# Performance work log

Measured on AMD Instinct MI355X. Metric: run time of the kernel, lower is better.

Reference implementation:

```python
import jax, jax.numpy as jnp
import numpy as np
import itertools

DIM = 576; HEADS = 18; HD = 32; WS = 7; H = 28; W = 28; EPS = 1e-5

def _bias_idxs(ws):
    pts = list(itertools.product(range(ws), range(ws)))
    offs = {}
    idxs = []
    for p1 in pts:
        for p2 in pts:
            o = (abs(p1[0] - p2[0]), abs(p1[1] - p2[1]))
            if o not in offs:
                offs[o] = len(offs)
            idxs.append(offs[o])
    return np.array(idxs, np.int32).reshape(len(pts), len(pts))

BIAS_IDXS = _bias_idxs(WS)          # [49, 49]
N_OFF = int(BIAS_IDXS.max()) + 1    # 49 distinct offsets

def _ln(x, g, b):
    m = x.mean(-1, keepdims=True)
    v = ((x - m) ** 2).mean(-1, keepdims=True)
    return (x - m) * jax.lax.rsqrt(v + EPS) * g + b

def setup_inputs() -> dict:
    key = jax.random.key(0)
    ks = jax.random.split(key, 10)
    B = 32; L = H * W; C = DIM; hid = 4 * C
    s = 0.02
    return {
        'x': jax.random.normal(ks[0], (B, L, C), jnp.float32),
        'ln1_g': jnp.ones((C,), jnp.float32),
        'ln1_b': jnp.zeros((C,), jnp.float32),
        'qkv_w': jax.random.normal(ks[1], (C, 3 * C), jnp.float32) * s,
        'qkv_b': jnp.zeros((3 * C,), jnp.float32),
        'attn_biases': jax.random.normal(ks[2], (HEADS, N_OFF), jnp.float32) * s,
        'proj_w': jax.random.normal(ks[3], (C, C), jnp.float32) * s,
        'proj_b': jnp.zeros((C,), jnp.float32),
        'conv_w': jax.random.normal(ks[4], (C, 1, 3, 3), jnp.float32) * 0.1,
        'bn_g': jnp.ones((C,), jnp.float32),
        'bn_b': jnp.zeros((C,), jnp.float32),
        'bn_mean': jax.random.normal(ks[5], (C,), jnp.float32) * 0.1,
        'bn_var': jax.random.uniform(ks[6], (C,), jnp.float32, 0.5, 1.5),
        'ln2_g': jnp.ones((C,), jnp.float32),
        'ln2_b': jnp.zeros((C,), jnp.float32),
        'fc1_w': jax.random.normal(ks[7], (C, hid), jnp.float32) * s,
        'fc1_b': jnp.zeros((hid,), jnp.float32),
        'fc2_w': jax.random.normal(ks[8], (hid, C), jnp.float32) * s,
        'fc2_b': jnp.zeros((C,), jnp.float32),
    }

def reference(x, ln1_g, ln1_b, qkv_w, qkv_b, attn_biases, proj_w, proj_b,
              conv_w, bn_g, bn_b, bn_mean, bn_var, ln2_g, ln2_b,
              fc1_w, fc1_b, fc2_w, fc2_b):
    B, L, C = x.shape
    nH, nW = H // WS, W // WS
    Nw = WS * WS
    scale = HD ** -0.5
    res = x
    # window partition: [B,L,C] -> [B*nH*nW, WS*WS, C] (H,W divisible by WS -> no pad)
    xw = x.reshape(B, nH, WS, nW, WS, C).transpose(0, 1, 3, 2, 4, 5).reshape(-1, Nw, C)
    h = _ln(xw, ln1_g, ln1_b)
    qkv = (h @ qkv_w + qkv_b).reshape(-1, Nw, HEADS, 3 * HD)
    q, k, v = qkv[..., :HD], qkv[..., HD:2 * HD], qkv[..., 2 * HD:]
    bias = attn_biases[:, BIAS_IDXS]  # gather -> [HEADS, Nw, Nw]
    scores = jnp.einsum('bnhd,bmhd->bhnm', q, k) * scale + bias[None]
    a = jax.nn.softmax(scores, axis=-1)
    o = jnp.einsum('bhnm,bmhd->bnhd', a, v).reshape(-1, Nw, C)
    o = o @ proj_w + proj_b
    # window reverse
    o = o.reshape(B, nH, nW, WS, WS, C).transpose(0, 1, 3, 2, 4, 5).reshape(B, L, C)
    x = res + o
    # depthwise 3x3 conv + BatchNorm (eval mode, running stats)
    xc = x.transpose(0, 2, 1).reshape(B, C, H, W)
    y = jax.lax.conv_general_dilated(xc, conv_w, (1, 1), ((1, 1), (1, 1)),
                                     feature_group_count=C,
                                     dimension_numbers=('NCHW', 'OIHW', 'NCHW'))
    inv = jax.lax.rsqrt(bn_var + EPS)
    y = (y - bn_mean[None, :, None, None]) * (inv * bn_g)[None, :, None, None] + bn_b[None, :, None, None]
    x = y.reshape(B, C, L).transpose(0, 2, 1)
    # MLP with pre-LayerNorm (exact GELU, matching torch nn.GELU)
    hm = _ln(x, ln2_g, ln2_b)
    hm = jax.nn.gelu(hm @ fc1_w + fc1_b, approximate=False)
    x = x + (hm @ fc2_w + fc2_b)
    return x
```

## Files before the change

kernel.cpp:

```cpp
#include <hip/hip_runtime.h>
#include <hip/hip_bf16.h>

typedef __attribute__((ext_vector_type(8))) short bf16x8;
typedef __attribute__((ext_vector_type(4))) float f32x4;

static __device__ __forceinline__ void stf(float* p, size_t i, float v) { p[i] = v; }
static __device__ __forceinline__ void stf(__hip_bfloat16* p, size_t i, float v) { p[i] = __float2bfloat16(v); }

static __device__ __forceinline__ void gload_lds16(const void* g, void* l) {
  __builtin_amdgcn_global_load_lds((const __attribute__((address_space(1))) void*)g,
                                   (__attribute__((address_space(3))) void*)l, 16, 0, 0);
}

__global__ void wt_kernel(const float* __restrict__ W, __hip_bfloat16* __restrict__ WT, int K, int N) {
  __shared__ float tile[32][33];
  const int kb = blockIdx.y * 32, nb = blockIdx.x * 32;
  const int tx = threadIdx.x & 31, ty = threadIdx.x >> 5;
#pragma unroll
  for (int i = 0; i < 4; ++i)
    tile[ty + i * 8][tx] = W[(size_t)(kb + ty + i * 8) * N + nb + tx];
  __syncthreads();
#pragma unroll
  for (int i = 0; i < 4; ++i)
    WT[(size_t)(nb + ty + i * 8) * K + kb + tx] = __float2bfloat16(tile[tx][ty + i * 8]);
}

__global__ void convprep_kernel(const float* __restrict__ w, const float* __restrict__ bng,
                                const float* __restrict__ bnb, const float* __restrict__ bnm,
                                const float* __restrict__ bnv, float* __restrict__ wT,
                                float* __restrict__ st) {
  const int i = blockIdx.x * 256 + threadIdx.x;
  if (i < 576 * 9) {
    const int t = i / 576, c = i - t * 576;
    wT[i] = w[c * 9 + t];
  }
  if (i < 576) {
    const float s = rsqrtf(bnv[i] + 1e-5f) * bng[i];
    st[i] = s;
    st[576 + i] = bnb[i] - bnm[i] * s;
  }
}

__global__ void ln_bf16_kernel(const float* __restrict__ x, const float* __restrict__ g,
                               const float* __restrict__ b, __hip_bfloat16* __restrict__ y) {
  const int row = blockIdx.x * 4 + (threadIdx.x >> 6);
  const int lane = threadIdx.x & 63;
  const float* p = x + (size_t)row * 576;
  float vals[9];
  float s = 0.f, ss = 0.f;
#pragma unroll
  for (int i = 0; i < 9; ++i) {
    float v = p[lane + i * 64];
    vals[i] = v; s += v; ss += v * v;
  }
#pragma unroll
  for (int o = 32; o; o >>= 1) { s += __shfl_down(s, o); ss += __shfl_down(ss, o); }
  s = __shfl(s, 0); ss = __shfl(ss, 0);
  const float m = s * (1.f / 576.f);
  const float rstd = rsqrtf(ss * (1.f / 576.f) - m * m + 1e-5f);
  __hip_bfloat16* q = y + (size_t)row * 576;
#pragma unroll
  for (int i = 0; i < 9; ++i) {
    const int c = lane + i * 64;
    q[c] = __float2bfloat16((vals[i] - m) * rstd * g[c] + b[c]);
  }
}

template <int EPI, typename TO>
__global__ __launch_bounds__(512, 1) void gemm_bt(
    const __hip_bfloat16* __restrict__ A, const __hip_bfloat16* __restrict__ BT,
    const float* __restrict__ bias, const float* __restrict__ res, TO* __restrict__ C,
    int M, int N, int K) {
  constexpr int BM = 256, BN = 192;
  constexpr int WM = 128, WN = 48;
  constexpr int MI = 8, NI = 3;
  constexpr int AI = 4, BI = 3;
  __shared__ __hip_bfloat16 sA[2][BM * 64];
  __shared__ __hip_bfloat16 sB[2][BN * 64];
  const int t = threadIdx.x;
  const int lane = t & 63;
  const int w = t >> 6;
  const int nwg = gridDim.x;
  const int qq = nwg >> 3, r = nwg & 7;
  const int xcd = blockIdx.x & 7, lidx = blockIdx.x >> 3;
  const int wgid = (xcd < r ? xcd * (qq + 1) : r * (qq + 1) + (xcd - r) * qq) + lidx;
  const int nx = N / BN;
  const int bm = (wgid / nx) * BM, bn = (wgid % nx) * BN;
  const int wm = (w >> 2) * WM, wn = (w & 3) * WN;
  const int l15 = lane & 15, l4 = lane >> 4;

  f32x4 acc[MI][NI];
#pragma unroll
  for (int mi = 0; mi < MI; ++mi)
#pragma unroll
    for (int ni = 0; ni < NI; ++ni) acc[mi][ni] = (f32x4){0.f, 0.f, 0.f, 0.f};

  const int wave_base = t & ~63;

  auto stage = [&](int buf, int kt) {
    const int k0 = kt << 6;
#pragma unroll
    for (int i = 0; i < AI; ++i) {
      const int slot = i * 512 + t;
      const int row = slot >> 3, kst = slot & 7;
      const int ksrc = kst ^ (row & 7);
      const __hip_bfloat16* g = A + (size_t)(bm + row) * K + k0 + ksrc * 8;
      gload_lds16(g, sA[buf] + (i * 512 + wave_base) * 8);
    }
#pragma unroll
    for (int i = 0; i < BI; ++i) {
      const int slot = i * 512 + t;
      const int row = slot >> 3, kst = slot & 7;
      const int ksrc = kst ^ (row & 7);
      const __hip_bfloat16* g = BT + (size_t)(bn + row) * K + k0 + ksrc * 8;
      gload_lds16(g, sB[buf] + (i * 512 + wave_base) * 8);
    }
  };

  auto compute = [&](int buf) {
    const __hip_bfloat16* pA = sA[buf];
    const __hip_bfloat16* pB = sB[buf];
#pragma unroll
    for (int kb = 0; kb < 2; ++kb) {
      bf16x8 a[MI], b[NI];
      const int kblk = kb * 4 + l4;
#pragma unroll
      for (int mi = 0; mi < MI; ++mi) {
        const int row = wm + mi * 16 + l15;
        a[mi] = *(const bf16x8*)(pA + row * 64 + ((kblk ^ (row & 7)) * 8));
      }
#pragma unroll
      for (int ni = 0; ni < NI; ++ni) {
        const int row = wn + ni * 16 + l15;
        b[ni] = *(const bf16x8*)(pB + row * 64 + ((kblk ^ (row & 7)) * 8));
      }
#pragma unroll
      for (int mi = 0; mi < MI; ++mi)
#pragma unroll
        for (int ni = 0; ni < NI; ++ni)
          acc[mi][ni] = __builtin_amdgcn_mfma_f32_16x16x32_bf16(a[mi], b[ni], acc[mi][ni], 0, 0, 0);
    }
  };

  const int nt = K >> 6;
  stage(0, 0);
  stage(1, 1);
  int cur = 0;
  for (int tt = 0; tt < nt; ++tt) {
    if (tt < nt - 1) asm volatile("s_waitcnt vmcnt(7)" ::: "memory");
    else             asm volatile("s_waitcnt vmcnt(0)" ::: "memory");
    __builtin_amdgcn_sched_barrier(0);
    __builtin_amdgcn_s_barrier();
    __builtin_amdgcn_sched_barrier(0);
    compute(cur);
    if (tt + 2 < nt) {
      __builtin_amdgcn_sched_barrier(0);
      __builtin_amdgcn_s_barrier();
      __builtin_amdgcn_sched_barrier(0);
      stage(cur, tt + 2);
    }
    cur ^= 1;
  }

#pragma unroll
  for (int mi = 0; mi < MI; ++mi) {
    const int mrow = bm + wm + mi * 16 + l4 * 4;
#pragma unroll
    for (int ni = 0; ni < NI; ++ni) {
      const int col = bn + wn + ni * 16 + l15;
      const float bv = bias[col];
#pragma unroll
      for (int r2 = 0; r2 < 4; ++r2) {
        const size_t idx = (size_t)(mrow + r2) * N + col;
        float v = acc[mi][ni][r2] + bv;
        if (EPI == 1) v += res[idx];
        if (EPI == 2) v = 0.5f * v * (1.0f + erff(v * 0.70710678118654752f));
        stf(C, idx, v);
      }
    }
  }
}

__global__ __launch_bounds__(64) void attn_mfma_kernel(
    const __hip_bfloat16* __restrict__ qkv, const float* __restrict__ biases,
    __hip_bfloat16* __restrict__ o) {
  __shared__ __hip_bfloat16 sQK[2][64][40];
  __shared__ __hip_bfloat16 sVT[32][72];
  __hip_bfloat16 (*sP)[72] = (__hip_bfloat16(*)[72])(&sQK[0][0][0]);

  const int wid  = blockIdx.x / 18;
  const int head = blockIdx.x - wid * 18;
  const int b  = wid >> 4;
  const int wi = wid & 15;
  const int wh = wi >> 2, wwc = wi & 3;
  const int lane = threadIdx.x;
  const int l15 = lane & 15, l4 = lane >> 4;

  {
    const __hip_bfloat16* basep = qkv + (size_t)head * 96;
    for (int idx = lane; idx < 49 * 12; idx += 64) {
      const int tkn = idx / 12, part = idx - tkn * 12;
      const int r = tkn / 7, c = tkn - r * 7;
      const size_t row = (size_t)b * 784 + (size_t)((wh * 7 + r) * 28 + wwc * 7 + c);
      bf16x8 v = *(const bf16x8*)(basep + row * 1728 + part * 8);
      if (part < 4)      *(bf16x8*)&sQK[0][tkn][part * 8] = v;
      else if (part < 8) *(bf16x8*)&sQK[1][tkn][(part - 4) * 8] = v;
      else {
        const int d0 = (part - 8) * 8;
        const short* sv = (const short*)&v;
#pragma unroll
        for (int e = 0; e < 8; ++e)
          sVT[d0 + e][tkn] = *(const __hip_bfloat16*)&sv[e];
      }
    }
    for (int idx = lane; idx < 32 * 15; idx += 64) {
      const int d = idx / 15, tt = 49 + (idx - d * 15);
      sVT[d][tt] = __float2bfloat16(0.0f);
    }
  }
  __syncthreads();

  f32x4 acc[4][4];
#pragma unroll
  for (int mi = 0; mi < 4; ++mi)
#pragma unroll
    for (int ni = 0; ni < 4; ++ni) acc[mi][ni] = (f32x4){0.f, 0.f, 0.f, 0.f};
  {
    bf16x8 aq[4], bk[4];
#pragma unroll
    for (int mi = 0; mi < 4; ++mi) aq[mi] = *(const bf16x8*)&sQK[0][mi * 16 + l15][l4 * 8];
#pragma unroll
    for (int ni = 0; ni < 4; ++ni) bk[ni] = *(const bf16x8*)&sQK[1][ni * 16 + l15][l4 * 8];
#pragma unroll
    for (int mi = 0; mi < 4; ++mi)
#pragma unroll
      for (int ni = 0; ni < 4; ++ni)
        acc[mi][ni] = __builtin_amdgcn_mfma_f32_16x16x32_bf16(aq[mi], bk[ni], acc[mi][ni], 0, 0, 0);
  }
  __syncthreads();

  const float scale = 0.17677669529663687f;
  const float* btab = biases + head * 49;
#pragma unroll
  for (int mi = 0; mi < 4; ++mi) {
#pragma unroll
    for (int rr = 0; rr < 4; ++rr) {
      const int i = mi * 16 + l4 * 4 + rr;
      const int ic = i < 49 ? i : 0;
      const int ri = ic / 7, ci = ic - ri * 7;
      float s[4];
#pragma unroll
      for (int ni = 0; ni < 4; ++ni) {
        const int j = ni * 16 + l15;
        if (j < 49) {
          const int rj = j / 7, cj = j - rj * 7;
          s[ni] = acc[mi][ni][rr] * scale + btab[__builtin_abs(ri - rj) * 7 + __builtin_abs(ci - cj)];
        } else {
          s[ni] = -1e30f;
        }
      }
      float m = fmaxf(fmaxf(s[0], s[1]), fmaxf(s[2], s[3]));
#pragma unroll
      for (int d = 1; d < 16; d <<= 1) m = fmaxf(m, __shfl_xor(m, d));
      float sum = 0.f;
#pragma unroll
      for (int ni = 0; ni < 4; ++ni) { s[ni] = __expf(s[ni] - m); sum += s[ni]; }
#pragma unroll
      for (int d = 1; d < 16; d <<= 1) sum += __shfl_xor(sum, d);
      const float inv = 1.0f / sum;
#pragma unroll
      for (int ni = 0; ni < 4; ++ni)
        sP[i][ni * 16 + l15] = __float2bfloat16(s[ni] * inv);
    }
  }
  __syncthreads();

  f32x4 oacc[4][2];
#pragma unroll
  for (int mi = 0; mi < 4; ++mi)
#pragma unroll
    for (int ni = 0; ni < 2; ++ni) oacc[mi][ni] = (f32x4){0.f, 0.f, 0.f, 0.f};
#pragma unroll
  for (int kb = 0; kb < 2; ++kb) {
    bf16x8 ap[4], bv[2];
#pragma unroll
    for (int mi = 0; mi < 4; ++mi) ap[mi] = *(const bf16x8*)&sP[mi * 16 + l15][kb * 32 + l4 * 8];
#pragma unroll
    for (int ni = 0; ni < 2; ++ni) bv[ni] = *(const bf16x8*)&sVT[ni * 16 + l15][kb * 32 + l4 * 8];
#pragma unroll
    for (int mi = 0; mi < 4; ++mi)
#pragma unroll
      for (int ni = 0; ni < 2; ++ni)
        oacc[mi][ni] = __builtin_amdgcn_mfma_f32_16x16x32_bf16(ap[mi], bv[ni], oacc[mi][ni], 0, 0, 0);
  }

#pragma unroll
  for (int mi = 0; mi < 4; ++mi) {
#pragma unroll
    for (int rr = 0; rr < 4; ++rr) {
      const int i = mi * 16 + l4 * 4 + rr;
      if (i < 49) {
        const int r = i / 7, c = i - r * 7;
        const size_t grow = (size_t)b * 784 + (size_t)((wh * 7 + r) * 28 + wwc * 7 + c);
#pragma unroll
        for (int ni = 0; ni < 2; ++ni)
          o[grow * 576 + head * 32 + ni * 16 + l15] = __float2bfloat16(oacc[mi][ni][rr]);
      }
    }
  }
}

__global__ void conv_bn_kernel(const float* __restrict__ x1, const float* __restrict__ wT,
                               const float* __restrict__ st, float* __restrict__ x2) {
  const size_t total = (size_t)32 * 784 * 144;
  const size_t idx = (size_t)blockIdx.x * 256 + threadIdx.x;
  if (idx >= total) return;
  const int c4 = (int)(idx % 144);
  const size_t p = idx / 144;
  const int pix = (int)(p % 784);
  const int b = (int)(p / 784);
  const int i = pix / 28, j = pix - (pix / 28) * 28;
  const int c = c4 * 4;
  f32x4 acc = (f32x4){0.f, 0.f, 0.f, 0.f};
#pragma unroll
  for (int dh = -1; dh <= 1; ++dh) {
#pragma unroll
    for (int dw = -1; dw <= 1; ++dw) {
      const int ii = i + dh, jj = j + dw;
      if (ii >= 0 && ii < 28 && jj >= 0 && jj < 28) {
        const f32x4 v = *(const f32x4*)&x1[((size_t)b * 784 + ii * 28 + jj) * 576 + c];
        const f32x4 wv = *(const f32x4*)&wT[((dh + 1) * 3 + (dw + 1)) * 576 + c];
        acc += v * wv;
      }
    }
  }
  const f32x4 s = *(const f32x4*)&st[c];
  const f32x4 tt = *(const f32x4*)&st[576 + c];
  *(f32x4*)&x2[((size_t)b * 784 + pix) * 576 + c] = acc * s + tt;
}

extern "C" void kernel_launch(void* const* d_in, const int* in_sizes, int n_in,
                              void* d_out, int out_size, void* d_ws, size_t ws_size,
                              hipStream_t stream) {
  (void)in_sizes; (void)n_in; (void)out_size; (void)ws_size;
  const float* x      = (const float*)d_in[0];
  const float* ln1g   = (const float*)d_in[1];
  const float* ln1b   = (const float*)d_in[2];
  const float* qkv_w  = (const float*)d_in[3];
  const float* qkv_b  = (const float*)d_in[4];
  const float* biases = (const float*)d_in[5];
  const float* proj_w = (const float*)d_in[6];
  const float* proj_b = (const float*)d_in[7];
  const float* conv_w = (const float*)d_in[8];
  const float* bng    = (const float*)d_in[9];
  const float* bnb    = (const float*)d_in[10];
  const float* bnm    = (const float*)d_in[11];
  const float* bnv    = (const float*)d_in[12];
  const float* ln2g   = (const float*)d_in[13];
  const float* ln2b   = (const float*)d_in[14];
  const float* fc1_w  = (const float*)d_in[15];
  const float* fc1_b  = (const float*)d_in[16];
  const float* fc2_w  = (const float*)d_in[17];
  const float* fc2_b  = (const float*)d_in[18];
  float* out = (float*)d_out;

  const int M = 25088;
  char* ws = (char*)d_ws;
  float* x2 = (float*)ws;
  char* regB = ws + 57802752;
  __hip_bfloat16* qkvb = (__hip_bfloat16*)regB;
  float*          x1   = (float*)regB;
  __hip_bfloat16* hm   = (__hip_bfloat16*)regB;
  char* regC = ws + 173408256;
  __hip_bfloat16* xn1  = (__hip_bfloat16*)regC;
  __hip_bfloat16* obuf = (__hip_bfloat16*)regC;
  __hip_bfloat16* xn2  = (__hip_bfloat16*)regC;
  char* regD = ws + 202309632;
  __hip_bfloat16* qkvT = (__hip_bfloat16*)regD;
  __hip_bfloat16* projT = (__hip_bfloat16*)(regD + 1990656);
  __hip_bfloat16* fc1T  = (__hip_bfloat16*)(regD + 1990656 + 663552);
  __hip_bfloat16* fc2T  = (__hip_bfloat16*)(regD + 1990656 + 663552 + 2654208);
  float* convT = (float*)(ws + 210272256);
  float* convST = convT + 9 * 576;

  wt_kernel<<<dim3(1728 / 32, 576 / 32), 256, 0, stream>>>(qkv_w, qkvT, 576, 1728);
  wt_kernel<<<dim3(576 / 32, 576 / 32), 256, 0, stream>>>(proj_w, projT, 576, 576);
  wt_kernel<<<dim3(2304 / 32, 576 / 32), 256, 0, stream>>>(fc1_w, fc1T, 576, 2304);
  wt_kernel<<<dim3(576 / 32, 2304 / 32), 256, 0, stream>>>(fc2_w, fc2T, 2304, 576);
  convprep_kernel<<<(576 * 9 + 255) / 256, 256, 0, stream>>>(conv_w, bng, bnb, bnm, bnv, convT, convST);

  ln_bf16_kernel<<<M / 4, 256, 0, stream>>>(x, ln1g, ln1b, xn1);
  gemm_bt<0, __hip_bfloat16><<<98 * 9, 512, 0, stream>>>(xn1, qkvT, qkv_b, nullptr, qkvb, M, 1728, 576);
  attn_mfma_kernel<<<512 * 18, 64, 0, stream>>>(qkvb, biases, obuf);
  gemm_bt<1, float><<<98 * 3, 512, 0, stream>>>(obuf, projT, proj_b, x, x1, M, 576, 576);
  conv_bn_kernel<<<(32 * 784 * 144 + 255) / 256, 256, 0, stream>>>(x1, convT, convST, x2);
  ln_bf16_kernel<<<M / 4, 256, 0, stream>>>(x2, ln2g, ln2b, xn2);
  gemm_bt<2, __hip_bfloat16><<<98 * 12, 512, 0, stream>>>(xn2, fc1T, fc1_b, nullptr, hm, M, 2304, 576);
  gemm_bt<1, float><<<98 * 3, 512, 0, stream>>>(hm, fc2T, fc2_b, x2, out, M, 576, 2304);
}
```

Before: 561.8 us.

## Add ping-pong GEMM with 2 blocks/CU and interleaved staging for QKV and FC1

Adds a new GEMM kernel that requests two workgroups per CU through launch bounds and splits each K-tile into four phases. Each phase interleaves LDS fragment loads and partial global-to-LDS prefetches with half of the MFMA work, separated by barriers and s_setprio. The goal is to overlap memory traffic with matrix math across the two co-resident blocks in ping-pong fashion. LDS use is 112 KB per block, so two blocks per CU may not fit, and the extra barriers add sync overhead; only the QKV and FC1 GEMMs switch to this kernel.

```diff
diff --git a/kernel.cpp b/kernel.cpp
--- a/kernel.cpp
+++ b/kernel.cpp
@@ -10,6 +10,17 @@
 static __device__ __forceinline__ void gload_lds16(const void* g, void* l) {
   __builtin_amdgcn_global_load_lds((const __attribute__((address_space(1))) void*)g,
                                    (__attribute__((address_space(3))) void*)l, 16, 0, 0);
+}
+static __device__ __forceinline__ void vm2() { asm volatile("s_waitcnt vmcnt(2)" ::: "memory"); }
+static __device__ __forceinline__ void vm0() { asm volatile("s_waitcnt vmcnt(0)" ::: "memory"); }
+static __device__ __forceinline__ void lgkm0() {
+  asm volatile("s_waitcnt lgkmcnt(0)" ::: "memory");
+  __builtin_amdgcn_sched_barrier(0);
+}
+static __device__ __forceinline__ void barrier() {
+  __builtin_amdgcn_sched_barrier(0);
+  __builtin_amdgcn_s_barrier();
+  __builtin_amdgcn_sched_barrier(0);
 }
 
 __global__ void wt_kernel(const float* __restrict__ W, __hip_bfloat16* __restrict__ WT, int K, int N) {
@@ -67,12 +78,130 @@
 }
 
 template <int EPI, typename TO>
+__global__ __launch_bounds__(512, 2) void gemm8(
+    const __hip_bfloat16* __restrict__ A, const __hip_bfloat16* __restrict__ BT,
+    const float* __restrict__ bias, const float* __restrict__ res, TO* __restrict__ C,
+    int M, int N, int K) {
+  constexpr int BM = 256, BN = 192;
+  __shared__ __hip_bfloat16 sA[2][BM * 64];
+  __shared__ __hip_bfloat16 sB[2][BN * 64];
+  const int t = threadIdx.x;
+  const int lane = t & 63;
+  const int w = t >> 6;
+  const int nwg = gridDim.x;
+  const int qq = nwg >> 3, r = nwg & 7;
+  const int xcd = blockIdx.x & 7, lidx = blockIdx.x >> 3;
+  const int wgid = (xcd < r ? xcd * (qq + 1) : r * (qq + 1) + (xcd - r) * qq) + lidx;
+  const int nx = N / BN;
+  const int bm = (wgid / nx) * BM, bn = (wgid % nx) * BN;
+  const int wm = (w >> 2) * 128, wn = (w & 3) * 48;
+  const int l15 = lane & 15, l4 = lane >> 4;
+  const int wave_base = t & ~63;
+
+  f32x4 acc[8][3];
+#pragma unroll
+  for (int mi = 0; mi < 8; ++mi)
+#pragma unroll
+    for (int ni = 0; ni < 3; ++ni) acc[mi][ni] = (f32x4){0.f, 0.f, 0.f, 0.f};
+
+  auto stA = [&](int buf, int kt, int u) {
+    const int slot = u * 512 + t;
+    const int row = slot >> 3, kst = slot & 7;
+    const int ksrc = kst ^ (row & 7);
+    gload_lds16(A + (size_t)(bm + row) * K + (kt << 6) + ksrc * 8,
+                sA[buf] + (u * 512 + wave_base) * 8);
+  };
+  auto stB = [&](int buf, int kt, int u) {
+    const int slot = u * 512 + t;
+    const int row = slot >> 3, kst = slot & 7;
+    const int ksrc = kst ^ (row & 7);
+    gload_lds16(BT + (size_t)(bn + row) * K + (kt << 6) + ksrc * 8,
+                sB[buf] + (u * 512 + wave_base) * 8);
+  };
+
+  bf16x8 a[4], b[3];
+  auto lda = [&](int c, int kb, int mh) {
+#pragma unroll
+    for (int i = 0; i < 4; ++i) {
+      const int row = wm + (mh * 4 + i) * 16 + l15;
+      const int kblk = kb * 4 + l4;
+      a[i] = *(const bf16x8*)(&sA[c][row * 64 + ((kblk ^ (row & 7)) * 8)]);
+    }
+  };
+  auto ldb = [&](int c, int kb) {
+#pragma unroll
+    for (int ni = 0; ni < 3; ++ni) {
+      const int row = wn + ni * 16 + l15;
+      const int kblk = kb * 4 + l4;
+      b[ni] = *(const bf16x8*)(&sB[c][row * 64 + ((kblk ^ (row & 7)) * 8)]);
+    }
+  };
+  auto mm = [&](int mh) {
+#pragma unroll
+    for (int i = 0; i < 4; ++i)
+#pragma unroll
+      for (int ni = 0; ni < 3; ++ni)
+        acc[mh * 4 + i][ni] =
+            __builtin_amdgcn_mfma_f32_16x16x32_bf16(a[i], b[ni], acc[mh * 4 + i][ni], 0, 0, 0);
+  };
+
+  stB(0, 0, 0); stB(0, 0, 1); stB(0, 0, 2);
+  stA(0, 0, 0); stA(0, 0, 2); stA(0, 0, 1); stA(0, 0, 3);
+
+  const int nt = K >> 6;
+  for (int tt = 0; tt < nt; ++tt) {
+    const int c = tt & 1, n1 = c ^ 1;
+    const int kt1 = tt + 1;
+    const bool pre = kt1 < nt;
+    vm2();
+    barrier();
+    lda(c, 0, 0); ldb(c, 0);
+    if (pre) { stB(n1, kt1, 0); stB(n1, kt1, 1); }
+    barrier(); lgkm0();
+    __builtin_amdgcn_s_setprio(1); mm(0); __builtin_amdgcn_s_setprio(0);
+    if (pre) vm2(); else vm0();
+    barrier();
+    lda(c, 0, 1);
+    if (pre) { stB(n1, kt1, 2); stA(n1, kt1, 0); }
+    barrier(); lgkm0();
+    __builtin_amdgcn_s_setprio(1); mm(1); __builtin_amdgcn_s_setprio(0);
+    barrier();
+    lda(c, 1, 0); ldb(c, 1);
+    if (pre) { stA(n1, kt1, 2); stA(n1, kt1, 1); }
+    barrier(); lgkm0();
+    __builtin_amdgcn_s_setprio(1); mm(0); __builtin_amdgcn_s_setprio(0);
+    barrier();
+    lda(c, 1, 1);
+    if (pre) { stA(n1, kt1, 3); }
+    barrier(); lgkm0();
+    __builtin_amdgcn_s_setprio(1); mm(1); __builtin_amdgcn_s_setprio(0);
+  }
+
+#pragma unroll
+  for (int mi = 0; mi < 8; ++mi) {
+    const int mrow = bm + wm + mi * 16 + l4 * 4;
+#pragma unroll
+    for (int ni = 0; ni < 3; ++ni) {
+      const int col = bn + wn + ni * 16 + l15;
+      const float bv = bias[col];
+#pragma unroll
+      for (int r2 = 0; r2 < 4; ++r2) {
+        const size_t idx = (size_t)(mrow + r2) * N + col;
+        float v = acc[mi][ni][r2] + bv;
+        if (EPI == 1) v += res[idx];
+        if (EPI == 2) v = 0.5f * v * (1.0f + erff(v * 0.70710678118654752f));
+        stf(C, idx, v);
+      }
+    }
+  }
+}
+
+template <int EPI, typename TO>
 __global__ __launch_bounds__(512, 1) void gemm_bt(
     const __hip_bfloat16* __restrict__ A, const __hip_bfloat16* __restrict__ BT,
     const float* __restrict__ bias, const float* __restrict__ res, TO* __restrict__ C,
     int M, int N, int K) {
   constexpr int BM = 256, BN = 192;
-  constexpr int WM = 128, WN = 48;
   constexpr int MI = 8, NI = 3;
   constexpr int AI = 4, BI = 3;
   __shared__ __hip_bfloat16 sA[2][BM * 64];
@@ -86,7 +215,7 @@
   const int wgid = (xcd < r ? xcd * (qq + 1) : r * (qq + 1) + (xcd - r) * qq) + lidx;
   const int nx = N / BN;
   const int bm = (wgid / nx) * BM, bn = (wgid % nx) * BN;
-  const int wm = (w >> 2) * WM, wn = (w & 3) * WN;
+  const int wm = (w >> 2) * 128, wn = (w & 3) * 48;
   const int l15 = lane & 15, l4 = lane >> 4;
 
   f32x4 acc[MI][NI];
@@ -104,16 +233,14 @@
       const int slot = i * 512 + t;
       const int row = slot >> 3, kst = slot & 7;
       const int ksrc = kst ^ (row & 7);
-      const __hip_bfloat16* g = A + (size_t)(bm + row) * K + k0 + ksrc * 8;
-      gload_lds16(g, sA[buf] + (i * 512 + wave_base) * 8);
+      gload_lds16(A + (size_t)(bm + row) * K + k0 + ksrc * 8, sA[buf] + (i * 512 + wave_base) * 8);
     }
 #pragma unroll
     for (int i = 0; i < BI; ++i) {
       const int slot = i * 512 + t;
       const int row = slot >> 3, kst = slot & 7;
       const int ksrc = kst ^ (row & 7);
-      const __hip_bfloat16* g = BT + (size_t)(bn + row) * K + k0 + ksrc * 8;
-      gload_lds16(g, sB[buf] + (i * 512 + wave_base) * 8);
+      gload_lds16(BT + (size_t)(bn + row) * K + k0 + ksrc * 8, sB[buf] + (i * 512 + wave_base) * 8);
     }
   };
 
@@ -149,14 +276,10 @@
   for (int tt = 0; tt < nt; ++tt) {
     if (tt < nt - 1) asm volatile("s_waitcnt vmcnt(7)" ::: "memory");
     else             asm volatile("s_waitcnt vmcnt(0)" ::: "memory");
-    __builtin_amdgcn_sched_barrier(0);
-    __builtin_amdgcn_s_barrier();
-    __builtin_amdgcn_sched_barrier(0);
+    barrier();
     compute(cur);
     if (tt + 2 < nt) {
-      __builtin_amdgcn_sched_barrier(0);
-      __builtin_amdgcn_s_barrier();
-      __builtin_amdgcn_sched_barrier(0);
+      barrier();
       stage(cur, tt + 2);
     }
     cur ^= 1;
@@ -390,11 +513,11 @@
   convprep_kernel<<<(576 * 9 + 255) / 256, 256, 0, stream>>>(conv_w, bng, bnb, bnm, bnv, convT, convST);
 
   ln_bf16_kernel<<<M / 4, 256, 0, stream>>>(x, ln1g, ln1b, xn1);
-  gemm_bt<0, __hip_bfloat16><<<98 * 9, 512, 0, stream>>>(xn1, qkvT, qkv_b, nullptr, qkvb, M, 1728, 576);
+  gemm8<0, __hip_bfloat16><<<98 * 9, 512, 0, stream>>>(xn1, qkvT, qkv_b, nullptr, qkvb, M, 1728, 576);
   attn_mfma_kernel<<<512 * 18, 64, 0, stream>>>(qkvb, biases, obuf);
   gemm_bt<1, float><<<98 * 3, 512, 0, stream>>>(obuf, projT, proj_b, x, x1, M, 576, 576);
   conv_bn_kernel<<<(32 * 784 * 144 + 255) / 256, 256, 0, stream>>>(x1, convT, convST, x2);
   ln_bf16_kernel<<<M / 4, 256, 0, stream>>>(x2, ln2g, ln2b, xn2);
-  gemm_bt<2, __hip_bfloat16><<<98 * 12, 512, 0, stream>>>(xn2, fc1T, fc1_b, nullptr, hm, M, 2304, 576);
+  gemm8<2, __hip_bfloat16><<<98 * 12, 512, 0, stream>>>(xn2, fc1T, fc1_b, nullptr, hm, M, 2304, 576);
   gemm_bt<1, float><<<98 * 3, 512, 0, stream>>>(hm, fc2T, fc2_b, x2, out, M, 576, 2304);
 }
```

New measurement: 561.1 us. No clear change (-0.1%).

## Add LDS-free direct-load GEMM for QKV, FC1 and FC2 projections

Applied to the files above, without the earlier changes.

Adds a gemm_direct kernel that loads A and B fragments straight from global memory into registers, with no LDS staging or barriers, using 128x192 tiles and 256-thread blocks. It replaces the LDS double-buffered 256x192 gemm_bt for the QKV, FC1 and FC2 GEMMs. The intent is to cut barrier and LDS overhead and raise occupancy with smaller tiles. The cost is that data is no longer shared between waves through LDS, so global/L2 traffic rises and the loads are strided per row.

```diff
diff --git a/kernel.cpp b/kernel.cpp
--- a/kernel.cpp
+++ b/kernel.cpp
@@ -10,6 +10,11 @@
 static __device__ __forceinline__ void gload_lds16(const void* g, void* l) {
   __builtin_amdgcn_global_load_lds((const __attribute__((address_space(1))) void*)g,
                                    (__attribute__((address_space(3))) void*)l, 16, 0, 0);
+}
+static __device__ __forceinline__ void barrier() {
+  __builtin_amdgcn_sched_barrier(0);
+  __builtin_amdgcn_s_barrier();
+  __builtin_amdgcn_sched_barrier(0);
 }
 
 __global__ void wt_kernel(const float* __restrict__ W, __hip_bfloat16* __restrict__ WT, int K, int N) {
@@ -67,12 +72,76 @@
 }
 
 template <int EPI, typename TO>
+__global__ __launch_bounds__(256) void gemm_direct(
+    const __hip_bfloat16* __restrict__ A, const __hip_bfloat16* __restrict__ BT,
+    const float* __restrict__ bias, const float* __restrict__ res, TO* __restrict__ C,
+    int M, int N, int K) {
+  const int t = threadIdx.x, lane = t & 63, w = t >> 6;
+  const int nwg = gridDim.x;
+  const int qq = nwg >> 3, r8 = nwg & 7;
+  const int xcd = blockIdx.x & 7, lidx = blockIdx.x >> 3;
+  const int wgid = (xcd < r8 ? xcd * (qq + 1) : r8 * (qq + 1) + (xcd - r8) * qq) + lidx;
+  const int nx = N / 192;
+  const int bm = (wgid / nx) * 128, bn = (wgid % nx) * 192;
+  const int wm = (w >> 1) * 64, wn = (w & 1) * 96;
+  const int l15 = lane & 15, l4 = lane >> 4;
+
+  f32x4 acc[4][6];
+#pragma unroll
+  for (int mi = 0; mi < 4; ++mi)
+#pragma unroll
+    for (int ni = 0; ni < 6; ++ni) acc[mi][ni] = (f32x4){0.f, 0.f, 0.f, 0.f};
+
+  const __hip_bfloat16* pa[4];
+  const __hip_bfloat16* pb[6];
+#pragma unroll
+  for (int mi = 0; mi < 4; ++mi)
+    pa[mi] = A + (size_t)(bm + wm + mi * 16 + l15) * K + l4 * 8;
+#pragma unroll
+  for (int ni = 0; ni < 6; ++ni)
+    pb[ni] = BT + (size_t)(bn + wn + ni * 16 + l15) * K + l4 * 8;
+
+  const int nk = K >> 5;
+#pragma unroll 2
+  for (int kt = 0; kt < nk; ++kt) {
+    bf16x8 a[4], b[6];
+    const int ko = kt * 32;
+#pragma unroll
+    for (int mi = 0; mi < 4; ++mi) a[mi] = *(const bf16x8*)(pa[mi] + ko);
+#pragma unroll
+    for (int ni = 0; ni < 6; ++ni) b[ni] = *(const bf16x8*)(pb[ni] + ko);
+#pragma unroll
+    for (int mi = 0; mi < 4; ++mi)
+#pragma unroll
+      for (int ni = 0; ni < 6; ++ni)
+        acc[mi][ni] = __builtin_amdgcn_mfma_f32_16x16x32_bf16(a[mi], b[ni], acc[mi][ni], 0, 0, 0);
+  }
+
+#pragma unroll
+  for (int mi = 0; mi < 4; ++mi) {
+    const int mrow = bm + wm + mi * 16 + l4 * 4;
+#pragma unroll
+    for (int ni = 0; ni < 6; ++ni) {
+      const int col = bn + wn + ni * 16 + l15;
+      const float bv = bias[col];
+#pragma unroll
+      for (int r2 = 0; r2 < 4; ++r2) {
+        const size_t idx = (size_t)(mrow + r2) * N + col;
+        float v = acc[mi][ni][r2] + bv;
+        if (EPI == 1) v += res[idx];
+        if (EPI == 2) v = 0.5f * v * (1.0f + erff(v * 0.70710678118654752f));
+        stf(C, idx, v);
+      }
+    }
+  }
+}
+
+template <int EPI, typename TO>
 __global__ __launch_bounds__(512, 1) void gemm_bt(
     const __hip_bfloat16* __restrict__ A, const __hip_bfloat16* __restrict__ BT,
     const float* __restrict__ bias, const float* __restrict__ res, TO* __restrict__ C,
     int M, int N, int K) {
   constexpr int BM = 256, BN = 192;
-  constexpr int WM = 128, WN = 48;
   constexpr int MI = 8, NI = 3;
   constexpr int AI = 4, BI = 3;
   __shared__ __hip_bfloat16 sA[2][BM * 64];
@@ -86,7 +155,7 @@
   const int wgid = (xcd < r ? xcd * (qq + 1) : r * (qq + 1) + (xcd - r) * qq) + lidx;
   const int nx = N / BN;
   const int bm = (wgid / nx) * BM, bn = (wgid % nx) * BN;
-  const int wm = (w >> 2) * WM, wn = (w & 3) * WN;
+  const int wm = (w >> 2) * 128, wn = (w & 3) * 48;
   const int l15 = lane & 15, l4 = lane >> 4;
 
   f32x4 acc[MI][NI];
@@ -104,16 +173,14 @@
       const int slot = i * 512 + t;
       const int row = slot >> 3, kst = slot & 7;
       const int ksrc = kst ^ (row & 7);
-      const __hip_bfloat16* g = A + (size_t)(bm + row) * K + k0 + ksrc * 8;
-      gload_lds16(g, sA[buf] + (i * 512 + wave_base) * 8);
+      gload_lds16(A + (size_t)(bm + row) * K + k0 + ksrc * 8, sA[buf] + (i * 512 + wave_base) * 8);
     }
 #pragma unroll
     for (int i = 0; i < BI; ++i) {
       const int slot = i * 512 + t;
       const int row = slot >> 3, kst = slot & 7;
       const int ksrc = kst ^ (row & 7);
-      const __hip_bfloat16* g = BT + (size_t)(bn + row) * K + k0 + ksrc * 8;
-      gload_lds16(g, sB[buf] + (i * 512 + wave_base) * 8);
+      gload_lds16(BT + (size_t)(bn + row) * K + k0 + ksrc * 8, sB[buf] + (i * 512 + wave_base) * 8);
     }
   };
 
@@ -149,14 +216,10 @@
   for (int tt = 0; tt < nt; ++tt) {
     if (tt < nt - 1) asm volatile("s_waitcnt vmcnt(7)" ::: "memory");
     else             asm volatile("s_waitcnt vmcnt(0)" ::: "memory");
-    __builtin_amdgcn_sched_barrier(0);
-    __builtin_amdgcn_s_barrier();
-    __builtin_amdgcn_sched_barrier(0);
+    barrier();
     compute(cur);
     if (tt + 2 < nt) {
-      __builtin_amdgcn_sched_barrier(0);
-      __builtin_amdgcn_s_barrier();
-      __builtin_amdgcn_sched_barrier(0);
+      barrier();
       stage(cur, tt + 2);
     }
     cur ^= 1;
@@ -390,11 +453,11 @@
   convprep_kernel<<<(576 * 9 + 255) / 256, 256, 0, stream>>>(conv_w, bng, bnb, bnm, bnv, convT, convST);
 
   ln_bf16_kernel<<<M / 4, 256, 0, stream>>>(x, ln1g, ln1b, xn1);
-  gemm_bt<0, __hip_bfloat16><<<98 * 9, 512, 0, stream>>>(xn1, qkvT, qkv_b, nullptr, qkvb, M, 1728, 576);
+  gemm_direct<0, __hip_bfloat16><<<196 * 9, 256, 0, stream>>>(xn1, qkvT, qkv_b, nullptr, qkvb, M, 1728, 576);
   attn_mfma_kernel<<<512 * 18, 64, 0, stream>>>(qkvb, biases, obuf);
   gemm_bt<1, float><<<98 * 3, 512, 0, stream>>>(obuf, projT, proj_b, x, x1, M, 576, 576);
   conv_bn_kernel<<<(32 * 784 * 144 + 255) / 256, 256, 0, stream>>>(x1, convT, convST, x2);
   ln_bf16_kernel<<<M / 4, 256, 0, stream>>>(x2, ln2g, ln2b, xn2);
-  gemm_bt<2, __hip_bfloat16><<<98 * 12, 512, 0, stream>>>(xn2, fc1T, fc1_b, nullptr, hm, M, 2304, 576);
-  gemm_bt<1, float><<<98 * 3, 512, 0, stream>>>(hm, fc2T, fc2_b, x2, out, M, 576, 2304);
-}
+  gemm_direct<2, __hip_bfloat16><<<196 * 12, 256, 0, stream>>>(xn2, fc1T, fc1_b, nullptr, hm, M, 2304, 576);
+  gemm_direct<1, float><<<196 * 3, 256, 0, stream>>>(hm, fc2T, fc2_b, x2, out, M, 576, 2304);
+}
```

After: 929.7 us. 65.5% more time.
